# Kernel tuning notes

Hardware: AMD Instinct MI355X
Metric: run time of the kernel (lower is better)

## Reference

```python
import jax, jax.numpy as jnp
import numpy as np

OUT_F, IN_F, RANK = 4096, 4096, 32
N_TOK = 8192  # batch 4 * seq 2048, flattened


def setup_inputs() -> dict:
    key = jax.random.key(0)
    k_x, k_w, k_s, k_a, k_b, k_bias = jax.random.split(key, 6)
    x = jax.random.normal(k_x, (N_TOK, IN_F), dtype=jnp.float32)
    # ternary weights in {-1, 0, +1}, stored as int8 buffer
    weight_q = (jax.random.randint(k_w, (OUT_F, IN_F), 0, 3) - 1).astype(jnp.int8)
    # per-output-channel absmean scale, shape [out, 1], positive
    scale = 0.02 + 0.05 * jax.random.uniform(k_s, (OUT_F, 1), dtype=jnp.float32)
    lora_A = 0.01 * jax.random.normal(k_a, (OUT_F, RANK), dtype=jnp.float32)
    lora_B = 0.01 * jax.random.normal(k_b, (RANK, IN_F), dtype=jnp.float32)
    bias = 0.01 * jax.random.normal(k_bias, (OUT_F,), dtype=jnp.float32)
    return {"x": x, "weight_q": weight_q, "scale": scale,
            "lora_A": lora_A, "lora_B": lora_B, "bias": bias}


def reference(x, weight_q, scale, lora_A, lora_B, bias):
    # out = (x @ W_q^T) * scale_per_out_channel + x @ B^T @ A^T + bias
    Wq = weight_q.astype(x.dtype)                       # dequantize {-1,0,1}
    out = jnp.einsum('ti,oi->to', x, Wq) * scale.reshape(1, -1)
    # low-rank LoRA residual: (x @ B^T) @ A^T, rank-RANK bottleneck
    out = out + (x @ lora_B.T) @ lora_A.T
    out = out + bias
    return out
```

## Files before the change

kernel.cpp:

```cpp
#include <hip/hip_runtime.h>
#include <stdint.h>

typedef unsigned short u16;
typedef __attribute__((ext_vector_type(8))) __bf16 bf16x8;
typedef __attribute__((ext_vector_type(4))) float f32x4;

__device__ __forceinline__ u16 f2bf(float f) {
  unsigned int u = __builtin_bit_cast(unsigned int, f);
  u = (u + 0x7FFFu + ((u >> 16) & 1u)) >> 16;
  return (u16)u;
}
__device__ __forceinline__ u16 tern2bf(int s) {
  return s == 0 ? (u16)0 : (s > 0 ? (u16)0x3F80 : (u16)0xBF80);
}

#define GLOAD_LDS16(g, l)                                                          \
  __builtin_amdgcn_global_load_lds((__attribute__((address_space(1))) void*)(g),   \
                                   (__attribute__((address_space(3))) void*)(l),   \
                                   16, 0, 0)

#define M_TOK 8192
#define N_OUT 4096
#define K_IN  4096
#define RANK  32

#define WS_XB    0ull
#define WS_WB    67108864ull
#define WS_BB    100663296ull
#define WS_A32   100925440ull
#define WS_T32   101187584ull
#define WS_TPART 101711872ull
#define WS_FLAG  110100480ull

__global__ void k_convert_x(const float4* __restrict__ x, ushort4* __restrict__ xb, int n4) {
  int stride = gridDim.x * blockDim.x;
  for (int i = blockIdx.x * blockDim.x + threadIdx.x; i < n4; i += stride) {
    float4 v = x[i];
    ushort4 o;
    o.x = f2bf(v.x); o.y = f2bf(v.y); o.z = f2bf(v.z); o.w = f2bf(v.w);
    xb[i] = o;
  }
}

__global__ void k_detect_wtype(const int* __restrict__ w, int* __restrict__ flag) {
  int v = w[threadIdx.x];
  bool ok = (v >= -1 && v <= 1);
  unsigned long long m = __ballot(ok);
  if (threadIdx.x == 0) *flag = (m == ~0ull) ? 1 : 0;
}

__global__ void k_convert_w(const void* __restrict__ wq, const int* __restrict__ flag,
                            ushort4* __restrict__ wb, int n4) {
  int is32 = *flag;
  int stride = gridDim.x * blockDim.x;
  for (int i = blockIdx.x * blockDim.x + threadIdx.x; i < n4; i += stride) {
    int s0, s1, s2, s3;
    if (is32) {
      int4 c = ((const int4*)wq)[i];
      s0 = c.x; s1 = c.y; s2 = c.z; s3 = c.w;
    } else {
      char4 c = ((const char4*)wq)[i];
      s0 = c.x; s1 = c.y; s2 = c.z; s3 = c.w;
    }
    ushort4 o;
    o.x = tern2bf(s0); o.y = tern2bf(s1); o.z = tern2bf(s2); o.w = tern2bf(s3);
    wb[i] = o;
  }
}

__global__ void k_prep_B(const float* __restrict__ loraB, u16* __restrict__ bb) {
  int idx = blockIdx.x * blockDim.x + threadIdx.x;
  if (idx < RANK * K_IN) bb[idx] = f2bf(loraB[idx]);
}

__global__ void k_prep_A(const float* __restrict__ loraA, const float* __restrict__ scale,
                         u16* __restrict__ a32) {
  int idx = blockIdx.x * blockDim.x + threadIdx.x;
  if (idx >= N_OUT * RANK) return;
  int o = idx >> 5;
  a32[idx] = f2bf(loraA[idx] / scale[o]);
}

__global__ __launch_bounds__(256) void k_lora_T(const u16* __restrict__ xb,
                                                const u16* __restrict__ bb,
                                                float* __restrict__ tpart) {
  __shared__ u16 As[256 * 32];
  __shared__ u16 Bs[32 * 32];
  int mt = blockIdx.x >> 3;
  int ks = blockIdx.x & 7;
  int tid = threadIdx.x, lane = tid & 63, wave = tid >> 6;
  int m0 = mt * 256;
  int kbase0 = ks * 512;
  f32x4 acc[4][2] = {};
  for (int step = 0; step < 16; ++step) {
    int kb = kbase0 + step * 32;
    __syncthreads();
#pragma unroll
    for (int i = 0; i < 4; ++i) {
      const u16* src = xb + (size_t)(m0 + i * 64 + (tid >> 2)) * K_IN + kb + (tid & 3) * 8;
      GLOAD_LDS16(src, &As[i * 2048 + tid * 8]);
    }
    if (tid < 128) {
      const u16* src = bb + (size_t)(tid >> 2) * K_IN + kb + (tid & 3) * 8;
      GLOAD_LDS16(src, &Bs[tid * 8]);
    }
    __syncthreads();
    bf16x8 b[2];
#pragma unroll
    for (int ni = 0; ni < 2; ++ni)
      b[ni] = *(const bf16x8*)&Bs[(ni * 16 + (lane & 15)) * 32 + (lane >> 4) * 8];
#pragma unroll
    for (int mi = 0; mi < 4; ++mi) {
      bf16x8 a = *(const bf16x8*)&As[(wave * 64 + mi * 16 + (lane & 15)) * 32 + (lane >> 4) * 8];
      acc[mi][0] = __builtin_amdgcn_mfma_f32_16x16x32_bf16(a, b[0], acc[mi][0], 0, 0, 0);
      acc[mi][1] = __builtin_amdgcn_mfma_f32_16x16x32_bf16(a, b[1], acc[mi][1], 0, 0, 0);
    }
  }
#pragma unroll
  for (int mi = 0; mi < 4; ++mi)
#pragma unroll
    for (int ni = 0; ni < 2; ++ni)
#pragma unroll
      for (int r = 0; r < 4; ++r) {
        int row = m0 + wave * 64 + mi * 16 + (lane >> 4) * 4 + r;
        int col = ni * 16 + (lane & 15);
        tpart[((size_t)ks * M_TOK + row) * RANK + col] = acc[mi][ni][r];
      }
}

__global__ void k_reduce_T(const float* __restrict__ tpart, u16* __restrict__ t32) {
  int idx = blockIdx.x * blockDim.x + threadIdx.x;
  if (idx >= M_TOK * RANK) return;
  int t = idx >> 5, r = idx & 31;
  float v = 0.f;
#pragma unroll
  for (int s = 0; s < 8; ++s) v += tpart[((size_t)s * M_TOK + t) * RANK + r];
  t32[idx] = f2bf(v);
}

__global__ __launch_bounds__(512, 2) void k_gemm8(const u16* __restrict__ xb,
                                                  const u16* __restrict__ wb,
                                                  const u16* __restrict__ t32,
                                                  const u16* __restrict__ a32,
                                                  const float* __restrict__ scale,
                                                  const float* __restrict__ bias,
                                                  float* __restrict__ out) {
  __shared__ u16 As[4][8192];
  __shared__ u16 Bs[4][8192];
  const int tid = threadIdx.x;
  const int l = tid & 63, w = tid >> 6;
  const int wm = w >> 2, wn = w & 3;
  const int bid = blockIdx.x;
  const int swz = (bid & 7) * 64 + (bid >> 3);
  const int m0 = (swz >> 4) * 256, n0 = (swz & 15) * 256;

  const int srow0 = (w * 2 + 0) * 16 + (l >> 2);
  const int srow1 = (w * 2 + 1) * 16 + (l >> 2);
  const int scx = ((l & 3) ^ ((l >> 3) & 3)) * 8;
  const int ldst0 = (w * 2 + 0) * 512 + l * 8;
  const int ldst1 = (w * 2 + 1) * 512 + l * 8;
  const int r15 = l & 15;
  const int cxr = (((l >> 4) ^ ((r15 >> 1) & 3)) * 8);

  f32x4 acc[8][4] = {};

  u16* AsF = &As[0][0];
  u16* BsF = &Bs[0][0];
  const u16* axs0 = xb + (size_t)(m0 + srow0) * K_IN + scx;
  const u16* axs1 = xb + (size_t)(m0 + srow1) * K_IN + scx;
  const u16* bxs0 = wb + (size_t)(n0 + srow0) * K_IN + scx;
  const u16* bxs1 = wb + (size_t)(n0 + srow1) * K_IN + scx;

#pragma unroll
  for (int ts = 0; ts < 3; ++ts) {
    GLOAD_LDS16(axs0 + ts * 32, AsF + ts * 8192 + ldst0);
    GLOAD_LDS16(axs1 + ts * 32, AsF + ts * 8192 + ldst1);
    GLOAD_LDS16(bxs0 + ts * 32, BsF + ts * 8192 + ldst0);
    GLOAD_LDS16(bxs1 + ts * 32, BsF + ts * 8192 + ldst1);
  }
  asm volatile("s_waitcnt vmcnt(4)" ::: "memory");
  asm volatile("s_barrier" ::: "memory");

  const int abase = (wm * 128 + r15) * 32 + cxr;
  const int bbase = (wn * 64 + r15) * 32 + cxr;

  const u16* ap0 = axs0 + 96;
  const u16* ap1 = axs1 + 96;
  const u16* bp0 = bxs0 + 96;
  const u16* bp1 = bxs1 + 96;

  bf16x8 fa0[4], fa1[4], fb[4];

#define SA(DST)                                                                     \
  { GLOAD_LDS16(ap0, AsF + (DST) * 8192 + ldst0);                                   \
    GLOAD_LDS16(ap1, AsF + (DST) * 8192 + ldst1);                                   \
    ap0 += 32; ap1 += 32; }
#define SB(DST)                                                                     \
  { GLOAD_LDS16(bp0, BsF + (DST) * 8192 + ldst0);                                   \
    GLOAD_LDS16(bp1, BsF + (DST) * 8192 + ldst1);                                   \
    bp0 += 32; bp1 += 32; }
#define W4  asm volatile("s_waitcnt vmcnt(4)" ::: "memory");
#define W0  asm volatile("s_waitcnt vmcnt(0)" ::: "memory");
#define BARR asm volatile("s_barrier" ::: "memory");
#define READN(NS)                                                                   \
  { const u16* An = AsF + (NS) * 8192;                                              \
    const u16* Bn = BsF + (NS) * 8192;                                              \
    _Pragma("unroll") for (int mi = 0; mi < 4; ++mi)                                \
        fa0[mi] = *(const bf16x8*)&An[abase + mi * 512];                            \
    _Pragma("unroll") for (int mi = 0; mi < 4; ++mi)                                \
        fa1[mi] = *(const bf16x8*)&An[abase + 2048 + mi * 512];                     \
    _Pragma("unroll") for (int nj = 0; nj < 4; ++nj)                                \
        fb[nj] = *(const bf16x8*)&Bn[bbase + nj * 512]; }

#define TILE(STAGE, WAIT, RD, BAR)                                                  \
  {                                                                                 \
    STAGE                                                                           \
    __builtin_amdgcn_s_setprio(1);                                                  \
    _Pragma("unroll") for (int mi = 0; mi < 4; ++mi)                                \
    _Pragma("unroll") for (int nj = 0; nj < 4; ++nj)                                \
        acc[mi][nj] =                                                               \
            __builtin_amdgcn_mfma_f32_16x16x32_bf16(fa0[mi], fb[nj], acc[mi][nj], 0, 0, 0); \
    _Pragma("unroll") for (int mi = 0; mi < 4; ++mi)                                \
    _Pragma("unroll") for (int nj = 0; nj < 4; ++nj)                                \
        acc[4 + mi][nj] =                                                           \
            __builtin_amdgcn_mfma_f32_16x16x32_bf16(fa1[mi], fb[nj], acc[4 + mi][nj], 0, 0, 0); \
    __builtin_amdgcn_s_setprio(0);                                                  \
    WAIT                                                                            \
    RD                                                                              \
    BAR                                                                             \
  }

  READN(0)

#pragma unroll 1
  for (int t = 0; t < 124; t += 4) {
    TILE(SA(3) SB(3), W4, READN(1), BARR)
    TILE(SA(0) SB(0), W4, READN(2), BARR)
    TILE(SA(1) SB(1), W4, READN(3), BARR)
    TILE(SA(2) SB(2), W4, READN(0), BARR)
  }
  TILE(SA(3) SB(3), W4, READN(1), BARR)
  {
    const u16* la0 = t32 + (size_t)(m0 + srow0) * RANK + scx;
    const u16* la1 = t32 + (size_t)(m0 + srow1) * RANK + scx;
    const u16* lb0 = a32 + (size_t)(n0 + srow0) * RANK + scx;
    const u16* lb1 = a32 + (size_t)(n0 + srow1) * RANK + scx;
    TILE({ GLOAD_LDS16(la0, AsF + 0 * 8192 + ldst0); GLOAD_LDS16(la1, AsF + 0 * 8192 + ldst1);
           GLOAD_LDS16(lb0, BsF + 0 * 8192 + ldst0); GLOAD_LDS16(lb1, BsF + 0 * 8192 + ldst1); },
         W4, READN(2), BARR)
  }
  TILE(, W0, READN(3), BARR)
  TILE(, , READN(0), BARR)
  TILE(, , , )

#pragma unroll
  for (int nj = 0; nj < 4; ++nj) {
    int col = n0 + wn * 64 + nj * 16 + r15;
    float s = scale[col], bv = bias[col];
#pragma unroll
    for (int fi = 0; fi < 8; ++fi) {
      int row = m0 + wm * 128 + (fi >> 2) * 64 + (fi & 3) * 16 + (l >> 4) * 4;
#pragma unroll
      for (int r = 0; r < 4; ++r)
        out[(size_t)(row + r) * N_OUT + col] = acc[fi][nj][r] * s + bv;
    }
  }
}

extern "C" void kernel_launch(void* const* d_in, const int* in_sizes, int n_in,
                              void* d_out, int out_size, void* d_ws, size_t ws_size,
                              hipStream_t stream) {
  const float* x     = (const float*)d_in[0];
  const void*  wq    = d_in[1];
  const float* scale = (const float*)d_in[2];
  const float* loraA = (const float*)d_in[3];
  const float* loraB = (const float*)d_in[4];
  const float* bias  = (const float*)d_in[5];
  float* out = (float*)d_out;

  char* ws = (char*)d_ws;
  u16*   xb    = (u16*)(ws + WS_XB);
  u16*   wbuf  = (u16*)(ws + WS_WB);
  u16*   bb    = (u16*)(ws + WS_BB);
  u16*   a32   = (u16*)(ws + WS_A32);
  u16*   t32   = (u16*)(ws + WS_T32);
  float* tpart = (float*)(ws + WS_TPART);
  int*   flag  = (int*)(ws + WS_FLAG);

  k_convert_x<<<2048, 256, 0, stream>>>((const float4*)x, (ushort4*)xb, M_TOK * K_IN / 4);
  k_detect_wtype<<<1, 64, 0, stream>>>((const int*)wq, flag);
  k_convert_w<<<2048, 256, 0, stream>>>(wq, flag, (ushort4*)wbuf, N_OUT * K_IN / 4);
  k_prep_B<<<512, 256, 0, stream>>>(loraB, bb);
  k_prep_A<<<512, 256, 0, stream>>>(loraA, scale, a32);
  k_lora_T<<<256, 256, 0, stream>>>(xb, bb, tpart);
  k_reduce_T<<<1024, 256, 0, stream>>>(tpart, t32);
  k_gemm8<<<512, 512, 0, stream>>>(xb, wbuf, t32, a32, scale, bias, out);

  (void)in_sizes; (void)n_in; (void)out_size; (void)ws_size;
}
```

Baseline: 310.9 us.

## Fuse x bf16 conversion with LoRA down-projection and merge small prep kernels

```diff
diff --git a/kernel.cpp b/kernel.cpp
--- a/kernel.cpp
+++ b/kernel.cpp
@@ -32,21 +32,27 @@
 #define WS_TPART 101711872ull
 #define WS_FLAG  110100480ull
 
-__global__ void k_convert_x(const float4* __restrict__ x, ushort4* __restrict__ xb, int n4) {
-  int stride = gridDim.x * blockDim.x;
-  for (int i = blockIdx.x * blockDim.x + threadIdx.x; i < n4; i += stride) {
-    float4 v = x[i];
-    ushort4 o;
-    o.x = f2bf(v.x); o.y = f2bf(v.y); o.z = f2bf(v.z); o.w = f2bf(v.w);
-    xb[i] = o;
-  }
-}
-
-__global__ void k_detect_wtype(const int* __restrict__ w, int* __restrict__ flag) {
-  int v = w[threadIdx.x];
-  bool ok = (v >= -1 && v <= 1);
-  unsigned long long m = __ballot(ok);
-  if (threadIdx.x == 0) *flag = (m == ~0ull) ? 1 : 0;
+__global__ __launch_bounds__(256) void k_prep(const int* __restrict__ wq,
+                                              const float* __restrict__ loraA,
+                                              const float* __restrict__ loraB,
+                                              const float* __restrict__ scale,
+                                              u16* __restrict__ bb,
+                                              u16* __restrict__ a32,
+                                              int* __restrict__ flag) {
+  if (blockIdx.x == 0 && threadIdx.x < 64) {
+    int v = wq[threadIdx.x];
+    bool ok = (v >= -1 && v <= 1);
+    unsigned long long m = __ballot(ok);
+    if (threadIdx.x == 0) *flag = (m == ~0ull) ? 1 : 0;
+  }
+  int idx = blockIdx.x * 256 + threadIdx.x;
+  if (blockIdx.x < 512) {
+    bb[idx] = f2bf(loraB[idx]);
+  } else {
+    int j = idx - 131072;
+    int o = j >> 5;
+    a32[j] = f2bf(loraA[j] / scale[o]);
+  }
 }
 
 __global__ void k_convert_w(const void* __restrict__ wq, const int* __restrict__ flag,
@@ -68,64 +74,89 @@
   }
 }
 
-__global__ void k_prep_B(const float* __restrict__ loraB, u16* __restrict__ bb) {
-  int idx = blockIdx.x * blockDim.x + threadIdx.x;
-  if (idx < RANK * K_IN) bb[idx] = f2bf(loraB[idx]);
-}
-
-__global__ void k_prep_A(const float* __restrict__ loraA, const float* __restrict__ scale,
-                         u16* __restrict__ a32) {
-  int idx = blockIdx.x * blockDim.x + threadIdx.x;
-  if (idx >= N_OUT * RANK) return;
-  int o = idx >> 5;
-  a32[idx] = f2bf(loraA[idx] / scale[o]);
-}
-
-__global__ __launch_bounds__(256) void k_lora_T(const u16* __restrict__ xb,
-                                                const u16* __restrict__ bb,
-                                                float* __restrict__ tpart) {
-  __shared__ u16 As[256 * 32];
-  __shared__ u16 Bs[32 * 32];
-  int mt = blockIdx.x >> 3;
-  int ks = blockIdx.x & 7;
-  int tid = threadIdx.x, lane = tid & 63, wave = tid >> 6;
-  int m0 = mt * 256;
-  int kbase0 = ks * 512;
-  f32x4 acc[4][2] = {};
-  for (int step = 0; step < 16; ++step) {
-    int kb = kbase0 + step * 32;
-    __syncthreads();
-#pragma unroll
-    for (int i = 0; i < 4; ++i) {
-      const u16* src = xb + (size_t)(m0 + i * 64 + (tid >> 2)) * K_IN + kb + (tid & 3) * 8;
-      GLOAD_LDS16(src, &As[i * 2048 + tid * 8]);
-    }
-    if (tid < 128) {
-      const u16* src = bb + (size_t)(tid >> 2) * K_IN + kb + (tid & 3) * 8;
-      GLOAD_LDS16(src, &Bs[tid * 8]);
-    }
-    __syncthreads();
-    bf16x8 b[2];
-#pragma unroll
-    for (int ni = 0; ni < 2; ++ni)
-      b[ni] = *(const bf16x8*)&Bs[(ni * 16 + (lane & 15)) * 32 + (lane >> 4) * 8];
-#pragma unroll
-    for (int mi = 0; mi < 4; ++mi) {
-      bf16x8 a = *(const bf16x8*)&As[(wave * 64 + mi * 16 + (lane & 15)) * 32 + (lane >> 4) * 8];
-      acc[mi][0] = __builtin_amdgcn_mfma_f32_16x16x32_bf16(a, b[0], acc[mi][0], 0, 0, 0);
-      acc[mi][1] = __builtin_amdgcn_mfma_f32_16x16x32_bf16(a, b[1], acc[mi][1], 0, 0, 0);
-    }
-  }
-#pragma unroll
-  for (int mi = 0; mi < 4; ++mi)
-#pragma unroll
-    for (int ni = 0; ni < 2; ++ni)
-#pragma unroll
-      for (int r = 0; r < 4; ++r) {
-        int row = m0 + wave * 64 + mi * 16 + (lane >> 4) * 4 + r;
-        int col = ni * 16 + (lane & 15);
-        tpart[((size_t)ks * M_TOK + row) * RANK + col] = acc[mi][ni][r];
+__global__ __launch_bounds__(256) void k_fused_xT(const float* __restrict__ x,
+                                                  const u16* __restrict__ bb,
+                                                  uint4* __restrict__ xb,
+                                                  float* __restrict__ tpart) {
+  __shared__ u16 Bs[32 * 512];
+  const int b = blockIdx.x;
+  const int ks = b & 7;
+  const int tg = b >> 3;
+  const int tid = threadIdx.x, l = tid & 63, wv = tid >> 6;
+
+#pragma unroll
+  for (int j = 0; j < 8; ++j) {
+    int i = j * 256 + tid;
+    int r = i >> 6, c = i & 63;
+    *(uint4*)&Bs[r * 512 + c * 8] =
+        *(const uint4*)&bb[(size_t)r * K_IN + ks * 512 + c * 8];
+  }
+  __syncthreads();
+
+  const int tbase = tg * 32 + wv * 8;
+#pragma unroll 1
+  for (int it = 0; it < 4; ++it) {
+    const int t = tbase + it * 2;
+    const float* xpA = x + (size_t)t * K_IN + ks * 512 + l * 8;
+    const float* xpB = xpA + K_IN;
+    float4 va0 = *(const float4*)xpA;
+    float4 va1 = *(const float4*)(xpA + 4);
+    float4 vb0 = *(const float4*)xpB;
+    float4 vb1 = *(const float4*)(xpB + 4);
+    u16 oA[8], oB[8];
+    oA[0] = f2bf(va0.x); oA[1] = f2bf(va0.y); oA[2] = f2bf(va0.z); oA[3] = f2bf(va0.w);
+    oA[4] = f2bf(va1.x); oA[5] = f2bf(va1.y); oA[6] = f2bf(va1.z); oA[7] = f2bf(va1.w);
+    oB[0] = f2bf(vb0.x); oB[1] = f2bf(vb0.y); oB[2] = f2bf(vb0.z); oB[3] = f2bf(vb0.w);
+    oB[4] = f2bf(vb1.x); oB[5] = f2bf(vb1.y); oB[6] = f2bf(vb1.z); oB[7] = f2bf(vb1.w);
+    uint4 pkA, pkB;
+    pkA.x = (unsigned)oA[0] | ((unsigned)oA[1] << 16);
+    pkA.y = (unsigned)oA[2] | ((unsigned)oA[3] << 16);
+    pkA.z = (unsigned)oA[4] | ((unsigned)oA[5] << 16);
+    pkA.w = (unsigned)oA[6] | ((unsigned)oA[7] << 16);
+    pkB.x = (unsigned)oB[0] | ((unsigned)oB[1] << 16);
+    pkB.y = (unsigned)oB[2] | ((unsigned)oB[3] << 16);
+    pkB.z = (unsigned)oB[4] | ((unsigned)oB[5] << 16);
+    pkB.w = (unsigned)oB[6] | ((unsigned)oB[7] << 16);
+    size_t xoff = ((size_t)t * K_IN + ks * 512 + l * 8) / 8;
+    xb[xoff] = pkA;
+    xb[xoff + K_IN / 8] = pkB;
+
+    float xfA[8], xfB[8];
+#pragma unroll
+    for (int j = 0; j < 8; ++j) {
+      xfA[j] = __builtin_bit_cast(float, ((unsigned)oA[j]) << 16);
+      xfB[j] = __builtin_bit_cast(float, ((unsigned)oB[j]) << 16);
+    }
+
+    float accA[32], accB[32];
+#pragma unroll
+    for (int r = 0; r < 32; ++r) { accA[r] = 0.f; accB[r] = 0.f; }
+#pragma unroll
+    for (int r = 0; r < 32; ++r) {
+      const uint4 braw = *(const uint4*)&Bs[r * 512 + l * 8];
+      const unsigned q[4] = {braw.x, braw.y, braw.z, braw.w};
+#pragma unroll
+      for (int p = 0; p < 4; ++p) {
+        float e0 = __builtin_bit_cast(float, q[p] << 16);
+        float e1 = __builtin_bit_cast(float, q[p] & 0xFFFF0000u);
+        accA[r] += xfA[2 * p] * e0 + xfA[2 * p + 1] * e1;
+        accB[r] += xfB[2 * p] * e0 + xfB[2 * p + 1] * e1;
       }
+    }
+#pragma unroll
+    for (int m = 1; m < 64; m <<= 1) {
+#pragma unroll
+      for (int r = 0; r < 32; ++r) {
+        accA[r] += __shfl_xor(accA[r], m, 64);
+        accB[r] += __shfl_xor(accB[r], m, 64);
+      }
+    }
+    if (l == 0) {
+      float* dA = tpart + ((size_t)ks * M_TOK + t) * RANK;
+#pragma unroll
+      for (int r = 0; r < 32; ++r) { dA[r] = accA[r]; dA[RANK + r] = accB[r]; }
+    }
+  }
 }
 
 __global__ void k_reduce_T(const float* __restrict__ tpart, u16* __restrict__ t32) {
@@ -287,12 +318,9 @@
   float* tpart = (float*)(ws + WS_TPART);
   int*   flag  = (int*)(ws + WS_FLAG);
 
-  k_convert_x<<<2048, 256, 0, stream>>>((const float4*)x, (ushort4*)xb, M_TOK * K_IN / 4);
-  k_detect_wtype<<<1, 64, 0, stream>>>((const int*)wq, flag);
+  k_prep<<<1024, 256, 0, stream>>>((const int*)wq, loraA, loraB, scale, bb, a32, flag);
   k_convert_w<<<2048, 256, 0, stream>>>(wq, flag, (ushort4*)wbuf, N_OUT * K_IN / 4);
-  k_prep_B<<<512, 256, 0, stream>>>(loraB, bb);
-  k_prep_A<<<512, 256, 0, stream>>>(loraA, scale, a32);
-  k_lora_T<<<256, 256, 0, stream>>>(xb, bb, tpart);
+  k_fused_xT<<<2048, 256, 0, stream>>>(x, bb, (uint4*)xb, tpart);
   k_reduce_T<<<1024, 256, 0, stream>>>(tpart, t32);
   k_gemm8<<<512, 512, 0, stream>>>(xb, wbuf, t32, a32, scale, bias, out);
 
```

Measured after the change: 535.8 us. 72.4% more time.

## Double GEMM workgroup to 1024 threads and merge small prep kernels

Applied to the files above, without the earlier changes.

```diff
diff --git a/kernel.cpp b/kernel.cpp
--- a/kernel.cpp
+++ b/kernel.cpp
@@ -32,6 +32,29 @@
 #define WS_TPART 101711872ull
 #define WS_FLAG  110100480ull
 
+__global__ __launch_bounds__(256) void k_prep(const int* __restrict__ wq,
+                                              const float* __restrict__ loraA,
+                                              const float* __restrict__ loraB,
+                                              const float* __restrict__ scale,
+                                              u16* __restrict__ bb,
+                                              u16* __restrict__ a32,
+                                              int* __restrict__ flag) {
+  if (blockIdx.x == 0 && threadIdx.x < 64) {
+    int v = wq[threadIdx.x];
+    bool ok = (v >= -1 && v <= 1);
+    unsigned long long m = __ballot(ok);
+    if (threadIdx.x == 0) *flag = (m == ~0ull) ? 1 : 0;
+  }
+  int idx = blockIdx.x * 256 + threadIdx.x;
+  if (blockIdx.x < 512) {
+    bb[idx] = f2bf(loraB[idx]);
+  } else {
+    int j = idx - 131072;
+    int o = j >> 5;
+    a32[j] = f2bf(loraA[j] / scale[o]);
+  }
+}
+
 __global__ void k_convert_x(const float4* __restrict__ x, ushort4* __restrict__ xb, int n4) {
   int stride = gridDim.x * blockDim.x;
   for (int i = blockIdx.x * blockDim.x + threadIdx.x; i < n4; i += stride) {
@@ -40,13 +63,6 @@
     o.x = f2bf(v.x); o.y = f2bf(v.y); o.z = f2bf(v.z); o.w = f2bf(v.w);
     xb[i] = o;
   }
-}
-
-__global__ void k_detect_wtype(const int* __restrict__ w, int* __restrict__ flag) {
-  int v = w[threadIdx.x];
-  bool ok = (v >= -1 && v <= 1);
-  unsigned long long m = __ballot(ok);
-  if (threadIdx.x == 0) *flag = (m == ~0ull) ? 1 : 0;
 }
 
 __global__ void k_convert_w(const void* __restrict__ wq, const int* __restrict__ flag,
@@ -66,19 +82,6 @@
     o.x = tern2bf(s0); o.y = tern2bf(s1); o.z = tern2bf(s2); o.w = tern2bf(s3);
     wb[i] = o;
   }
-}
-
-__global__ void k_prep_B(const float* __restrict__ loraB, u16* __restrict__ bb) {
-  int idx = blockIdx.x * blockDim.x + threadIdx.x;
-  if (idx < RANK * K_IN) bb[idx] = f2bf(loraB[idx]);
-}
-
-__global__ void k_prep_A(const float* __restrict__ loraA, const float* __restrict__ scale,
-                         u16* __restrict__ a32) {
-  int idx = blockIdx.x * blockDim.x + threadIdx.x;
-  if (idx >= N_OUT * RANK) return;
-  int o = idx >> 5;
-  a32[idx] = f2bf(loraA[idx] / scale[o]);
 }
 
 __global__ __launch_bounds__(256) void k_lora_T(const u16* __restrict__ xb,
@@ -138,13 +141,13 @@
   t32[idx] = f2bf(v);
 }
 
-__global__ __launch_bounds__(512, 2) void k_gemm8(const u16* __restrict__ xb,
-                                                  const u16* __restrict__ wb,
-                                                  const u16* __restrict__ t32,
-                                                  const u16* __restrict__ a32,
-                                                  const float* __restrict__ scale,
-                                                  const float* __restrict__ bias,
-                                                  float* __restrict__ out) {
+__global__ __launch_bounds__(1024, 4) void k_gemm8(const u16* __restrict__ xb,
+                                                   const u16* __restrict__ wb,
+                                                   const u16* __restrict__ t32,
+                                                   const u16* __restrict__ a32,
+                                                   const float* __restrict__ scale,
+                                                   const float* __restrict__ bias,
+                                                   float* __restrict__ out) {
   __shared__ u16 As[4][8192];
   __shared__ u16 Bs[4][8192];
   const int tid = threadIdx.x;
@@ -154,61 +157,45 @@
   const int swz = (bid & 7) * 64 + (bid >> 3);
   const int m0 = (swz >> 4) * 256, n0 = (swz & 15) * 256;
 
-  const int srow0 = (w * 2 + 0) * 16 + (l >> 2);
-  const int srow1 = (w * 2 + 1) * 16 + (l >> 2);
-  const int scx = ((l & 3) ^ ((l >> 3) & 3)) * 8;
-  const int ldst0 = (w * 2 + 0) * 512 + l * 8;
-  const int ldst1 = (w * 2 + 1) * 512 + l * 8;
+  const int srow = tid >> 2;
+  const int scx = ((tid & 3) ^ ((tid >> 3) & 3)) * 8;
+  const int ldst = tid * 8;
   const int r15 = l & 15;
   const int cxr = (((l >> 4) ^ ((r15 >> 1) & 3)) * 8);
 
-  f32x4 acc[8][4] = {};
+  f32x4 acc[4][4] = {};
 
   u16* AsF = &As[0][0];
   u16* BsF = &Bs[0][0];
-  const u16* axs0 = xb + (size_t)(m0 + srow0) * K_IN + scx;
-  const u16* axs1 = xb + (size_t)(m0 + srow1) * K_IN + scx;
-  const u16* bxs0 = wb + (size_t)(n0 + srow0) * K_IN + scx;
-  const u16* bxs1 = wb + (size_t)(n0 + srow1) * K_IN + scx;
+  const u16* axs = xb + (size_t)(m0 + srow) * K_IN + scx;
+  const u16* bxs = wb + (size_t)(n0 + srow) * K_IN + scx;
 
 #pragma unroll
   for (int ts = 0; ts < 3; ++ts) {
-    GLOAD_LDS16(axs0 + ts * 32, AsF + ts * 8192 + ldst0);
-    GLOAD_LDS16(axs1 + ts * 32, AsF + ts * 8192 + ldst1);
-    GLOAD_LDS16(bxs0 + ts * 32, BsF + ts * 8192 + ldst0);
-    GLOAD_LDS16(bxs1 + ts * 32, BsF + ts * 8192 + ldst1);
+    GLOAD_LDS16(axs + ts * 32, AsF + ts * 8192 + ldst);
+    GLOAD_LDS16(bxs + ts * 32, BsF + ts * 8192 + ldst);
   }
   asm volatile("s_waitcnt vmcnt(4)" ::: "memory");
   asm volatile("s_barrier" ::: "memory");
 
-  const int abase = (wm * 128 + r15) * 32 + cxr;
+  const int abase = (wm * 64 + r15) * 32 + cxr;
   const int bbase = (wn * 64 + r15) * 32 + cxr;
 
-  const u16* ap0 = axs0 + 96;
-  const u16* ap1 = axs1 + 96;
-  const u16* bp0 = bxs0 + 96;
-  const u16* bp1 = bxs1 + 96;
-
-  bf16x8 fa0[4], fa1[4], fb[4];
-
-#define SA(DST)                                                                     \
-  { GLOAD_LDS16(ap0, AsF + (DST) * 8192 + ldst0);                                   \
-    GLOAD_LDS16(ap1, AsF + (DST) * 8192 + ldst1);                                   \
-    ap0 += 32; ap1 += 32; }
-#define SB(DST)                                                                     \
-  { GLOAD_LDS16(bp0, BsF + (DST) * 8192 + ldst0);                                   \
-    GLOAD_LDS16(bp1, BsF + (DST) * 8192 + ldst1);                                   \
-    bp0 += 32; bp1 += 32; }
-#define W4  asm volatile("s_waitcnt vmcnt(4)" ::: "memory");
+  const u16* ap = axs + 96;
+  const u16* bp = bxs + 96;
+
+  bf16x8 fa[4], fb[4];
+
+#define SA(DST) { GLOAD_LDS16(ap, AsF + (DST) * 8192 + ldst); ap += 32; }
+#define SB(DST) { GLOAD_LDS16(bp, BsF + (DST) * 8192 + ldst); bp += 32; }
+#define W2  asm volatile("s_waitcnt vmcnt(2)" ::: "memory");
 #define W0  asm volatile("s_waitcnt vmcnt(0)" ::: "memory");
 #define BARR asm volatile("s_barrier" ::: "memory");
 #define READN(NS)                                                                   \
   { const u16* An = AsF + (NS) * 8192;                                              \
     const u16* Bn = BsF + (NS) * 8192;                                              \
     _Pragma("unroll") for (int mi = 0; mi < 4; ++mi)                                \
-        fa0[mi] = *(const bf16x8*)&An[abase + mi * 512];                            \
-    _Pragma("unroll") for (int mi = 0; mi < 4; ++mi)                                \
-        fa1[mi] = *(const bf16x8*)&An[abase + 2048 + mi * 512];                     \
+        fa[mi] = *(const bf16x8*)&An[abase + mi * 512];                             \
     _Pragma("unroll") for (int nj = 0; nj < 4; ++nj)                                \
         fb[nj] = *(const bf16x8*)&Bn[bbase + nj * 512]; }
 
@@ -219,11 +206,7 @@
     _Pragma("unroll") for (int mi = 0; mi < 4; ++mi)                                \
     _Pragma("unroll") for (int nj = 0; nj < 4; ++nj)                                \
         acc[mi][nj] =                                                               \
-            __builtin_amdgcn_mfma_f32_16x16x32_bf16(fa0[mi], fb[nj], acc[mi][nj], 0, 0, 0); \
-    _Pragma("unroll") for (int mi = 0; mi < 4; ++mi)                                \
-    _Pragma("unroll") for (int nj = 0; nj < 4; ++nj)                                \
-        acc[4 + mi][nj] =                                                           \
-            __builtin_amdgcn_mfma_f32_16x16x32_bf16(fa1[mi], fb[nj], acc[4 + mi][nj], 0, 0, 0); \
+            __builtin_amdgcn_mfma_f32_16x16x32_bf16(fa[mi], fb[nj], acc[mi][nj], 0, 0, 0); \
     __builtin_amdgcn_s_setprio(0);                                                  \
     WAIT                                                                            \
     RD                                                                              \
@@ -234,20 +217,17 @@
 
 #pragma unroll 1
   for (int t = 0; t < 124; t += 4) {
-    TILE(SA(3) SB(3), W4, READN(1), BARR)
-    TILE(SA(0) SB(0), W4, READN(2), BARR)
-    TILE(SA(1) SB(1), W4, READN(3), BARR)
-    TILE(SA(2) SB(2), W4, READN(0), BARR)
-  }
-  TILE(SA(3) SB(3), W4, READN(1), BARR)
+    TILE(SA(3) SB(3), W2, READN(1), BARR)
+    TILE(SA(0) SB(0), W2, READN(2), BARR)
+    TILE(SA(1) SB(1), W2, READN(3), BARR)
+    TILE(SA(2) SB(2), W2, READN(0), BARR)
+  }
+  TILE(SA(3) SB(3), W2, READN(1), BARR)
   {
-    const u16* la0 = t32 + (size_t)(m0 + srow0) * RANK + scx;
-    const u16* la1 = t32 + (size_t)(m0 + srow1) * RANK + scx;
-    const u16* lb0 = a32 + (size_t)(n0 + srow0) * RANK + scx;
-    const u16* lb1 = a32 + (size_t)(n0 + srow1) * RANK + scx;
-    TILE({ GLOAD_LDS16(la0, AsF + 0 * 8192 + ldst0); GLOAD_LDS16(la1, AsF + 0 * 8192 + ldst1);
-           GLOAD_LDS16(lb0, BsF + 0 * 8192 + ldst0); GLOAD_LDS16(lb1, BsF + 0 * 8192 + ldst1); },
-         W4, READN(2), BARR)
+    const u16* la = t32 + (size_t)(m0 + srow) * RANK + scx;
+    const u16* lb = a32 + (size_t)(n0 + srow) * RANK + scx;
+    TILE({ GLOAD_LDS16(la, AsF + 0 * 8192 + ldst); GLOAD_LDS16(lb, BsF + 0 * 8192 + ldst); },
+         W2, READN(2), BARR)
   }
   TILE(, W0, READN(3), BARR)
   TILE(, , READN(0), BARR)
@@ -258,11 +238,11 @@
     int col = n0 + wn * 64 + nj * 16 + r15;
     float s = scale[col], bv = bias[col];
 #pragma unroll
-    for (int fi = 0; fi < 8; ++fi) {
-      int row = m0 + wm * 128 + (fi >> 2) * 64 + (fi & 3) * 16 + (l >> 4) * 4;
+    for (int mi = 0; mi < 4; ++mi) {
+      int row = m0 + wm * 64 + mi * 16 + (l >> 4) * 4;
 #pragma unroll
       for (int r = 0; r < 4; ++r)
-        out[(size_t)(row + r) * N_OUT + col] = acc[fi][nj][r] * s + bv;
+        out[(size_t)(row + r) * N_OUT + col] = acc[mi][nj][r] * s + bv;
     }
   }
 }
@@ -287,14 +267,12 @@
   float* tpart = (float*)(ws + WS_TPART);
   int*   flag  = (int*)(ws + WS_FLAG);
 
+  k_prep<<<1024, 256, 0, stream>>>((const int*)wq, loraA, loraB, scale, bb, a32, flag);
   k_convert_x<<<2048, 256, 0, stream>>>((const float4*)x, (ushort4*)xb, M_TOK * K_IN / 4);
-  k_detect_wtype<<<1, 64, 0, stream>>>((const int*)wq, flag);
   k_convert_w<<<2048, 256, 0, stream>>>(wq, flag, (ushort4*)wbuf, N_OUT * K_IN / 4);
-  k_prep_B<<<512, 256, 0, stream>>>(loraB, bb);
-  k_prep_A<<<512, 256, 0, stream>>>(loraA, scale, a32);
   k_lora_T<<<256, 256, 0, stream>>>(xb, bb, tpart);
   k_reduce_T<<<1024, 256, 0, stream>>>(tpart, t32);
-  k_gemm8<<<512, 512, 0, stream>>>(xb, wbuf, t32, a32, scale, bias, out);
+  k_gemm8<<<512, 1024, 0, stream>>>(xb, wbuf, t32, a32, scale, bias, out);
 
   (void)in_sizes; (void)n_in; (void)out_size; (void)ws_size;
 }
```

Measured after the change: 320.2 us. 3.0% more time.
